# Performance work log

Hardware: AMD Instinct MI355X
Metric: run time of the kernel (lower is better)

## Reference

```python
import jax, jax.numpy as jnp
import numpy as np
from jax import lax

B, S, D, H, T = 128, 512, 128, 128, 20


def setup_inputs() -> dict:
    key = jax.random.key(0)
    ks = jax.random.split(key, 16)
    sc = 1.0 / np.sqrt(H)
    u = lambda k, shape: jax.random.uniform(k, shape, jnp.float32, -sc, sc)
    return {
        "inputs": jax.random.normal(ks[0], (B, S, D), jnp.float32),
        "tags": jax.random.randint(ks[1], (B, S), 0, T),
        "mask": jnp.ones((B, S), jnp.bool_),
        "w_ih_f": u(ks[2], (4 * H, D)),
        "w_hh_f": u(ks[3], (4 * H, H)),
        "b_f": u(ks[4], (4 * H,)),
        "w_ih_b": u(ks[5], (4 * H, D)),
        "w_hh_b": u(ks[6], (4 * H, H)),
        "b_b": u(ks[7], (4 * H,)),
        "w_out": u(ks[8], (T, 2 * H)),
        "b_out": u(ks[9], (T,)),
        "start_trans": jax.random.uniform(ks[10], (T,), jnp.float32, -0.1, 0.1),
        "end_trans": jax.random.uniform(ks[11], (T,), jnp.float32, -0.1, 0.1),
        "trans": jax.random.uniform(ks[12], (T, T), jnp.float32, -0.1, 0.1),
    }


def _lstm_dir(x, w_ih, w_hh, b, reverse):
    # x: [B,S,D] -> hidden states [B,S,H]
    xp = jnp.einsum('bsd,gd->bsg', x, w_ih) + b  # precomputed input gates [B,S,4H]
    if reverse:
        xp = xp[:, ::-1]
    h0 = jnp.zeros((x.shape[0], H), x.dtype)
    c0 = jnp.zeros((x.shape[0], H), x.dtype)

    def step(carry, xt):
        h, c = carry
        g = xt + h @ w_hh.T
        i, f, gg, o = jnp.split(g, 4, axis=-1)
        i, f, o = jax.nn.sigmoid(i), jax.nn.sigmoid(f), jax.nn.sigmoid(o)
        c = f * c + i * jnp.tanh(gg)
        h = o * jnp.tanh(c)
        return (h, c), h

    _, hs = lax.scan(step, (h0, c0), xp.transpose(1, 0, 2))
    hs = hs.transpose(1, 0, 2)  # [B,S,H]
    if reverse:
        hs = hs[:, ::-1]
    return hs


def _crf_nll(em, tags, mask, start_trans, end_trans, trans):
    # em: [B,S,T]; torchcrf log-likelihood, reduction='mean', negated
    b, s, t = em.shape
    maskf = mask.astype(em.dtype)
    batch = jnp.arange(b)
    # numerator: score of the gold path
    num = start_trans[tags[:, 0]] + em[batch, 0, tags[:, 0]]
    em_tag = jnp.take_along_axis(em, tags[:, :, None], axis=2)[:, :, 0]  # [B,S]
    trans_tag = trans[tags[:, :-1], tags[:, 1:]]  # [B,S-1]
    num = num + jnp.sum((trans_tag + em_tag[:, 1:]) * maskf[:, 1:], axis=1)
    seq_ends = jnp.sum(mask.astype(jnp.int32), axis=1) - 1
    num = num + end_trans[tags[batch, seq_ends]]
    # denominator: forward algorithm (logsumexp semiring) via scan
    score0 = start_trans[None, :] + em[:, 0]  # [B,T]

    def step(score, inp):
        em_t, m_t = inp
        nxt = jax.nn.logsumexp(score[:, :, None] + trans[None] + em_t[:, None, :], axis=1)
        return jnp.where(m_t[:, None], nxt, score), None

    score, _ = lax.scan(step, score0, (em[:, 1:].transpose(1, 0, 2), mask[:, 1:].T))
    den = jax.nn.logsumexp(score + end_trans[None, :], axis=1)
    return -jnp.mean(num - den)


def reference(inputs, tags, mask, w_ih_f, w_hh_f, b_f, w_ih_b, w_hh_b, b_b,
              w_out, b_out, start_trans, end_trans, trans):
    h_f = _lstm_dir(inputs, w_ih_f, w_hh_f, b_f, reverse=False)
    h_b = _lstm_dir(inputs, w_ih_b, w_hh_b, b_b, reverse=True)
    lstm_out = jnp.concatenate([h_f, h_b], axis=-1)  # [B,S,2H]
    emissions = jnp.einsum('bsh,th->bst', lstm_out, w_out) + b_out  # [B,S,T]
    return _crf_nll(emissions, tags, mask, start_trans, end_trans, trans)
```

## Files before the change

### kernel.cpp

```cpp
#include <hip/hip_runtime.h>
#include <cstdint>
#include <cstddef>

#define DEVINL __device__ __forceinline__

constexpr int Bz = 128, Sl = 512, Dm = 128, Hd = 128, NC = 1024, Tt = 20;
constexpr int Mrows = Bz * Sl;

constexpr size_t OFF_XP   = 17043456;
constexpr size_t OFF_HS   = 151261184;
constexpr size_t OFF_PART = 190058496;

DEVINL unsigned short f2bf(float f) {
    uint32_t u = __float_as_uint(f);
    u += 0x7fffu + ((u >> 16) & 1u);
    return (unsigned short)(u >> 16);
}
DEVINL float bf2f(unsigned short h) { return __uint_as_float(((uint32_t)h) << 16); }

DEVINL float rcpf(float x) { return __builtin_amdgcn_rcpf(x); }

DEVINL void barrier_lds_only() {
    __asm__ __volatile__("s_waitcnt lgkmcnt(0)" ::: "memory");
    __builtin_amdgcn_s_barrier();
    __asm__ __volatile__("" ::: "memory");
}

template <int CTRL>
DEVINL float qperm(float v) {
    int i = __float_as_int(v);
    int r = __builtin_amdgcn_update_dpp(i, i, CTRL, 0xF, 0xF, true);
    return __int_as_float(r);
}

typedef __attribute__((ext_vector_type(8))) __bf16 bf16x8;
typedef __attribute__((ext_vector_type(4))) float f32x4;
typedef _Float16 __attribute__((ext_vector_type(2))) half2_t;
typedef _Float16 __attribute__((ext_vector_type(8))) half8_t;

__global__ __launch_bounds__(256) void gemm_xp_k(
    const float* __restrict__ X, const float* __restrict__ wihf, const float* __restrict__ wihb,
    const float* __restrict__ b_f, const float* __restrict__ b_b,
    unsigned short* __restrict__ xp)
{
    __shared__ __align__(16) unsigned short As[128 * 72];
    __shared__ __align__(16) unsigned short Bs[128 * 72];
    const int m0 = blockIdx.x * 128, n0 = blockIdx.y * 128;
    const float* Bsrc = (n0 < 512) ? (wihf + (size_t)n0 * 128) : (wihb + (size_t)(n0 - 512) * 128);
    const int tid = threadIdx.x;
    const int wave = tid >> 6, lane = tid & 63;
    const int wm = (wave >> 1) * 64, wn = (wave & 1) * 64;
    const int ln = lane & 15, qd = lane >> 4;
    const int colc = (tid & 15) * 4, rowb = tid >> 4;

    f32x4 acc[4][4] = {};
    for (int ks = 0; ks < 2; ++ks) {
        const int k0 = ks * 64;
        __syncthreads();
        #pragma unroll
        for (int r = 0; r < 8; ++r) {
            int row = rowb + r * 16;
            float4 av = *(const float4*)(&X[(size_t)(m0 + row) * 128 + k0 + colc]);
            float4 bv = *(const float4*)(&Bsrc[(size_t)row * 128 + k0 + colc]);
            ushort4 au; au.x = f2bf(av.x); au.y = f2bf(av.y); au.z = f2bf(av.z); au.w = f2bf(av.w);
            ushort4 bu; bu.x = f2bf(bv.x); bu.y = f2bf(bv.y); bu.z = f2bf(bv.z); bu.w = f2bf(bv.w);
            *(ushort4*)(&As[row * 72 + colc]) = au;
            *(ushort4*)(&Bs[row * 72 + colc]) = bu;
        }
        __syncthreads();
        #pragma unroll
        for (int kk = 0; kk < 2; ++kk) {
            const int kb = kk * 32 + qd * 8;
            bf16x8 af[4], bfr[4];
            #pragma unroll
            for (int i = 0; i < 4; ++i) {
                af[i]  = *(const bf16x8*)(&As[(wm + i * 16 + ln) * 72 + kb]);
                bfr[i] = *(const bf16x8*)(&Bs[(wn + i * 16 + ln) * 72 + kb]);
            }
            #pragma unroll
            for (int i = 0; i < 4; ++i)
                #pragma unroll
                for (int j = 0; j < 4; ++j)
                    acc[i][j] = __builtin_amdgcn_mfma_f32_16x16x32_bf16(af[i], bfr[j], acc[i][j], 0, 0, 0);
        }
    }
    #pragma unroll
    for (int j = 0; j < 4; ++j) {
        const int col = n0 + wn + j * 16 + ln;
        const float bv = (col < 512) ? b_f[col] : b_b[col - 512];
        #pragma unroll
        for (int i = 0; i < 4; ++i) {
            const int rowg = m0 + wm + i * 16 + qd * 4;
            const int bidx = rowg >> 9, tloc = rowg & 511;
            ushort4 o;
            o.x = f2bf(acc[i][j][0] + bv); o.y = f2bf(acc[i][j][1] + bv);
            o.z = f2bf(acc[i][j][2] + bv); o.w = f2bf(acc[i][j][3] + bv);
            *(ushort4*)(xp + ((size_t)bidx * 1024 + col) * 512 + tloc) = o;
        }
    }
}

__global__ __launch_bounds__(512, 1) void lstm_k(
    const float* __restrict__ whf, const float* __restrict__ whb,
    const unsigned short* __restrict__ xp, unsigned short* __restrict__ hs)
{
    __shared__ __align__(16) _Float16 h_buf[2][128];
    const int dir = blockIdx.x >> 7;
    const int b   = blockIdx.x & 127;
    const int tid = threadIdx.x;
    const int lane = tid & 63;
    const int wv   = tid >> 6;
    const int q    = lane & 3;
    const int u    = wv * 16 + (lane >> 2);
    const int grow = q * 128 + u;

    const float* wsrc = dir ? whb : whf;
    half2_t w2[4][16];
    #pragma unroll
    for (int g = 0; g < 4; ++g) {
        const float* wrow = wsrc + (size_t)(g * 128 + u) * 128 + q * 32;
        #pragma unroll
        for (int k = 0; k < 16; ++k)
            w2[g][k] = half2_t{(_Float16)wrow[2 * k], (_Float16)wrow[2 * k + 1]};
    }

    const float S  = (q == 2) ? 2.f : 1.f;
    const float Aa = (q == 2) ? 2.f : 1.f;
    const float Bc = (q == 2) ? -1.f : 0.f;

    if (tid < 128) { h_buf[0][tid] = (_Float16)0.f; h_buf[1][tid] = (_Float16)0.f; }
    __syncthreads();

    const unsigned short* xrow = xp + ((size_t)b * 1024 + dir * 512 + grow) * 512;
    unsigned short* hptr = hs + (size_t)dir * Mrows * 128 + (size_t)b * Sl * 128 + u
                              + (dir ? (size_t)(Sl - 1) * 128 : 0);
    const int hstep = dir ? -128 : 128;

    float c = 0.f;
    ushort4 cur;
    {
        ushort4 r = *(const ushort4*)(xrow + (dir ? 508 : 0));
        cur = dir ? ushort4{r.w, r.z, r.y, r.x} : r;
    }

    for (int t = 0; t < Sl; t += 4) {
        const int tn = (t + 4 < Sl) ? (t + 4) : 0;
        ushort4 nraw = *(const ushort4*)(xrow + (dir ? (508 - tn) : tn));

        #pragma unroll
        for (int s = 0; s < 4; ++s) {
            const int p = s & 1;
            const unsigned short xb = (s == 0) ? cur.x : (s == 1) ? cur.y : (s == 2) ? cur.z : cur.w;
            float xv = bf2f(xb);

            const half8_t* hp = (const half8_t*)&h_buf[p][q * 32];
            float p0 = 0.f, p1 = 0.f, p2 = 0.f, p3 = 0.f;
            #pragma unroll
            for (int k = 0; k < 4; ++k) {
                half8_t hv = hp[k];
                const half2_t* h2 = (const half2_t*)&hv;
                #pragma unroll
                for (int j = 0; j < 4; ++j) {
                    p0 = __builtin_amdgcn_fdot2(w2[0][4 * k + j], h2[j], p0, false);
                    p1 = __builtin_amdgcn_fdot2(w2[1][4 * k + j], h2[j], p1, false);
                    p2 = __builtin_amdgcn_fdot2(w2[2][4 * k + j], h2[j], p2, false);
                    p3 = __builtin_amdgcn_fdot2(w2[3][4 * k + j], h2[j], p3, false);
                }
            }
            float keep0 = (q & 1) ? p1 : p0;
            float send0 = (q & 1) ? p0 : p1;
            float keep1 = (q & 1) ? p3 : p2;
            float send1 = (q & 1) ? p2 : p3;
            float s0 = keep0 + qperm<0xB1>(send0);
            float s1 = keep1 + qperm<0xB1>(send1);
            float keep2 = (q & 2) ? s1 : s0;
            float send2 = (q & 2) ? s0 : s1;
            float tot = keep2 + qperm<0x4E>(send2) + xv;

            float act = Aa * rcpf(1.f + __expf(-S * tot)) + Bc;
            float a0 = qperm<0x00>(act);
            float a1 = qperm<0x55>(act);
            float a2 = qperm<0xAA>(act);
            float a3 = qperm<0xFF>(act);
            c = fmaf(a1, c, a0 * a2);
            float th = 1.f - 2.f * rcpf(1.f + __expf(2.f * c));
            float h = a3 * th;
            if (q == 0) {
                _Float16 hh = (_Float16)h;
                h_buf[1 - p][u] = hh;
                unsigned short hbits; __builtin_memcpy(&hbits, &hh, 2);
                *hptr = hbits;
            }
            hptr += hstep;
            barrier_lds_only();
        }
        cur = dir ? ushort4{nraw.w, nraw.z, nraw.y, nraw.x} : nraw;
    }
}

__global__ __launch_bounds__(320, 1) void emcrf_k(
    const unsigned short* __restrict__ hs, const float* __restrict__ wout,
    const float* __restrict__ bout, const int* __restrict__ tags,
    const float* __restrict__ st, const float* __restrict__ et,
    const float* __restrict__ trans, float* __restrict__ part)
{
    __shared__ float em_s[Sl * Tt];
    __shared__ float red[320];
    const int b = blockIdx.x, tid = threadIdx.x, lane = tid & 63;
    const int* tg = tags + (size_t)b * Sl;

    {
        const int tag  = tid % 20;
        const int copy = tid / 20;
        const float* wr = wout + (size_t)tag * 256;
        half2_t wreg[128];
        #pragma unroll
        for (int k = 0; k < 128; ++k)
            wreg[k] = half2_t{(_Float16)wr[2 * k], (_Float16)wr[2 * k + 1]};
        const float bo = bout[tag];
        const unsigned short* hf_base = hs + (size_t)b * Sl * 128;
        const unsigned short* hb_base = hs + (size_t)Mrows * 128 + (size_t)b * Sl * 128;
        for (int i = 0; i < 32; ++i) {
            const int t = copy + 16 * i;
            const uint4* hf4 = (const uint4*)(hf_base + (size_t)t * 128);
            const uint4* hb4 = (const uint4*)(hb_base + (size_t)t * 128);
            float a0 = bo, a1 = 0.f, a2 = 0.f, a3 = 0.f;
            #pragma unroll
            for (int k = 0; k < 16; ++k) {
                uint4 v = hf4[k];
                half2_t h2[4]; __builtin_memcpy(h2, &v, 16);
                a0 = __builtin_amdgcn_fdot2(wreg[4 * k + 0], h2[0], a0, false);
                a1 = __builtin_amdgcn_fdot2(wreg[4 * k + 1], h2[1], a1, false);
                a2 = __builtin_amdgcn_fdot2(wreg[4 * k + 2], h2[2], a2, false);
                a3 = __builtin_amdgcn_fdot2(wreg[4 * k + 3], h2[3], a3, false);
            }
            #pragma unroll
            for (int k = 0; k < 16; ++k) {
                uint4 v = hb4[k];
                half2_t h2[4]; __builtin_memcpy(h2, &v, 16);
                a0 = __builtin_amdgcn_fdot2(wreg[64 + 4 * k + 0], h2[0], a0, false);
                a1 = __builtin_amdgcn_fdot2(wreg[64 + 4 * k + 1], h2[1], a1, false);
                a2 = __builtin_amdgcn_fdot2(wreg[64 + 4 * k + 2], h2[2], a2, false);
                a3 = __builtin_amdgcn_fdot2(wreg[64 + 4 * k + 3], h2[3], a3, false);
            }
            em_s[t * 20 + tag] = (a0 + a1) + (a2 + a3);
        }
    }
    __syncthreads();

    float nacc = 0.f;
    for (int t = 1 + tid; t < Sl; t += 320) {
        int tp = tg[t - 1], tc = tg[t];
        nacc += trans[tp * Tt + tc] + em_s[t * 20 + tc];
    }
    red[tid] = nacc;
    __syncthreads();

    if (tid < 64) {
        float v = red[lane] + red[lane + 64] + red[lane + 128] + red[lane + 192] + red[lane + 256];
        #pragma unroll
        for (int off = 32; off; off >>= 1) v += __shfl_down(v, off);

        float Etr[20];
        #pragma unroll
        for (int i = 0; i < 20; ++i)
            Etr[i] = (lane < 20) ? __expf(trans[i * Tt + lane]) : 0.f;

        float C = 0.f;
        float p = (lane < 20) ? __expf(st[lane] + em_s[lane]) : 0.f;
        float ev1 = (lane < 20) ? em_s[1 * 20 + lane] : 0.f;
        float ev2 = (lane < 20) ? em_s[2 * 20 + lane] : 0.f;
        for (int t = 1; t < Sl; ++t) {
            float ev = ev1;
            ev1 = ev2;
            int tn = t + 2 < Sl ? t + 2 : Sl - 1;
            ev2 = (lane < 20) ? em_s[tn * 20 + lane] : 0.f;

            float q0 = 0.f, q1 = 0.f, q2 = 0.f, q3 = 0.f;
            #pragma unroll
            for (int i = 0; i < 20; i += 4) {
                q0 = fmaf(__int_as_float(__builtin_amdgcn_readlane(__float_as_int(p), i + 0)), Etr[i + 0], q0);
                q1 = fmaf(__int_as_float(__builtin_amdgcn_readlane(__float_as_int(p), i + 1)), Etr[i + 1], q1);
                q2 = fmaf(__int_as_float(__builtin_amdgcn_readlane(__float_as_int(p), i + 2)), Etr[i + 2], q2);
                q3 = fmaf(__int_as_float(__builtin_amdgcn_readlane(__float_as_int(p), i + 3)), Etr[i + 3], q3);
            }
            p = ((q0 + q1) + (q2 + q3)) * __expf(ev);
            if ((t & 3) == 0) {
                float S0 = 0.f, S1 = 0.f, S2 = 0.f, S3 = 0.f;
                #pragma unroll
                for (int i = 0; i < 20; i += 4) {
                    S0 += __int_as_float(__builtin_amdgcn_readlane(__float_as_int(p), i + 0));
                    S1 += __int_as_float(__builtin_amdgcn_readlane(__float_as_int(p), i + 1));
                    S2 += __int_as_float(__builtin_amdgcn_readlane(__float_as_int(p), i + 2));
                    S3 += __int_as_float(__builtin_amdgcn_readlane(__float_as_int(p), i + 3));
                }
                float Ssum = (S0 + S1) + (S2 + S3);
                C += __logf(Ssum);
                p *= rcpf(Ssum);
            }
        }
        float f = (lane < 20) ? p * __expf(et[lane]) : 0.f;
        float S0 = 0.f, S1 = 0.f, S2 = 0.f, S3 = 0.f;
        #pragma unroll
        for (int i = 0; i < 20; i += 4) {
            S0 += __int_as_float(__builtin_amdgcn_readlane(__float_as_int(f), i + 0));
            S1 += __int_as_float(__builtin_amdgcn_readlane(__float_as_int(f), i + 1));
            S2 += __int_as_float(__builtin_amdgcn_readlane(__float_as_int(f), i + 2));
            S3 += __int_as_float(__builtin_amdgcn_readlane(__float_as_int(f), i + 3));
        }
        float den = C + __logf((S0 + S1) + (S2 + S3));
        if (lane == 0)
            part[b] = v + st[tg[0]] + em_s[tg[0]] + et[tg[Sl - 1]] - den;
    }
}

__global__ void fin_k(const float* __restrict__ part, float* __restrict__ out) {
    int l = threadIdx.x;
    float v = part[l] + part[l + 64];
    #pragma unroll
    for (int off = 32; off; off >>= 1) v += __shfl_xor(v, off);
    if (l == 0) out[0] = -v * (1.f / 128.f);
}

extern "C" void kernel_launch(void* const* d_in, const int* in_sizes, int n_in,
                              void* d_out, int out_size, void* d_ws, size_t ws_size,
                              hipStream_t stream) {
    const float* x      = (const float*)d_in[0];
    const int*   tags   = (const int*)d_in[1];
    const float* w_ih_f = (const float*)d_in[3];
    const float* w_hh_f = (const float*)d_in[4];
    const float* b_f    = (const float*)d_in[5];
    const float* w_ih_b = (const float*)d_in[6];
    const float* w_hh_b = (const float*)d_in[7];
    const float* b_b    = (const float*)d_in[8];
    const float* w_out  = (const float*)d_in[9];
    const float* b_out  = (const float*)d_in[10];
    const float* st     = (const float*)d_in[11];
    const float* et     = (const float*)d_in[12];
    const float* trans  = (const float*)d_in[13];
    float* out = (float*)d_out;

    char* ws = (char*)d_ws;
    unsigned short* xp   = (unsigned short*)(ws + OFF_XP);
    unsigned short* hs   = (unsigned short*)(ws + OFF_HS);
    float*          part = (float*)(ws + OFF_PART);

    gemm_xp_k<<<dim3(Mrows / 128, NC / 128), 256, 0, stream>>>(x, w_ih_f, w_ih_b, b_f, b_b, xp);
    lstm_k<<<256, 512, 0, stream>>>(w_hh_f, w_hh_b, xp, hs);
    emcrf_k<<<Bz, 320, 0, stream>>>(hs, w_out, b_out, tags, st, et, trans, part);
    fin_k<<<1, 64, 0, stream>>>(part, out);
}
```

Measured before the change: 553.1 us.

## Split emission and CRF kernels, restructure input GEMM to reuse A tile

The input-projection GEMM now loads each 64-row X tile once and loops over all eight 128-column weight tiles, instead of launching a 2D grid that reloads X per column tile. The fused emission+CRF kernel is split in two. The emission kernel runs 4 blocks per batch element, stages w_out through LDS and writes emissions to a global buffer. A single-wave CRF kernel then reads them with an 8-deep register prefetch. This spreads the emission dot products across more CUs and removes the 320-thread block that sat mostly idle during the serial CRF scan, at the cost of a global round-trip for emissions and an extra launch.

```diff
diff --git a/kernel.cpp b/kernel.cpp
--- a/kernel.cpp
+++ b/kernel.cpp
@@ -9,6 +9,7 @@
 
 constexpr size_t OFF_XP   = 17043456;
 constexpr size_t OFF_HS   = 151261184;
+constexpr size_t OFF_EM   = 184815616;
 constexpr size_t OFF_PART = 190058496;
 
 DEVINL unsigned short f2bf(float f) {
@@ -38,64 +39,73 @@
 typedef _Float16 __attribute__((ext_vector_type(2))) half2_t;
 typedef _Float16 __attribute__((ext_vector_type(8))) half8_t;
 
-__global__ __launch_bounds__(256) void gemm_xp_k(
+__global__ __launch_bounds__(256, 2) void gemm_xp_k(
     const float* __restrict__ X, const float* __restrict__ wihf, const float* __restrict__ wihb,
     const float* __restrict__ b_f, const float* __restrict__ b_b,
     unsigned short* __restrict__ xp)
 {
-    __shared__ __align__(16) unsigned short As[128 * 72];
-    __shared__ __align__(16) unsigned short Bs[128 * 72];
-    const int m0 = blockIdx.x * 128, n0 = blockIdx.y * 128;
-    const float* Bsrc = (n0 < 512) ? (wihf + (size_t)n0 * 128) : (wihb + (size_t)(n0 - 512) * 128);
+    __shared__ __align__(16) unsigned short As[64 * 132];
+    __shared__ __align__(16) unsigned short Bs[128 * 132];
+    const int m0 = blockIdx.x * 64;
     const int tid = threadIdx.x;
     const int wave = tid >> 6, lane = tid & 63;
-    const int wm = (wave >> 1) * 64, wn = (wave & 1) * 64;
+    const int wm = (wave >> 1) * 32, wn = (wave & 1) * 64;
     const int ln = lane & 15, qd = lane >> 4;
-    const int colc = (tid & 15) * 4, rowb = tid >> 4;
-
-    f32x4 acc[4][4] = {};
-    for (int ks = 0; ks < 2; ++ks) {
-        const int k0 = ks * 64;
+    const int colc = (tid & 31) * 4, rowb = tid >> 5;
+
+    #pragma unroll
+    for (int r = 0; r < 8; ++r) {
+        int row = rowb + r * 8;
+        float4 av = *(const float4*)(&X[(size_t)(m0 + row) * 128 + colc]);
+        ushort4 au; au.x = f2bf(av.x); au.y = f2bf(av.y); au.z = f2bf(av.z); au.w = f2bf(av.w);
+        *(ushort4*)(&As[row * 132 + colc]) = au;
+    }
+
+    const int bidx = m0 >> 9;
+    const int tbase = m0 & 511;
+
+    for (int nt = 0; nt < 8; ++nt) {
+        const float* Bsrc = (nt < 4) ? (wihf + (size_t)nt * 128 * 128)
+                                     : (wihb + (size_t)(nt - 4) * 128 * 128);
         __syncthreads();
         #pragma unroll
-        for (int r = 0; r < 8; ++r) {
-            int row = rowb + r * 16;
-            float4 av = *(const float4*)(&X[(size_t)(m0 + row) * 128 + k0 + colc]);
-            float4 bv = *(const float4*)(&Bsrc[(size_t)row * 128 + k0 + colc]);
-            ushort4 au; au.x = f2bf(av.x); au.y = f2bf(av.y); au.z = f2bf(av.z); au.w = f2bf(av.w);
+        for (int r = 0; r < 16; ++r) {
+            int row = rowb + r * 8;
+            float4 bv = *(const float4*)(&Bsrc[(size_t)row * 128 + colc]);
             ushort4 bu; bu.x = f2bf(bv.x); bu.y = f2bf(bv.y); bu.z = f2bf(bv.z); bu.w = f2bf(bv.w);
-            *(ushort4*)(&As[row * 72 + colc]) = au;
-            *(ushort4*)(&Bs[row * 72 + colc]) = bu;
+            *(ushort4*)(&Bs[row * 132 + colc]) = bu;
         }
         __syncthreads();
-        #pragma unroll
-        for (int kk = 0; kk < 2; ++kk) {
+
+        f32x4 acc[2][4] = {};
+        #pragma unroll
+        for (int kk = 0; kk < 4; ++kk) {
             const int kb = kk * 32 + qd * 8;
-            bf16x8 af[4], bfr[4];
-            #pragma unroll
-            for (int i = 0; i < 4; ++i) {
-                af[i]  = *(const bf16x8*)(&As[(wm + i * 16 + ln) * 72 + kb]);
-                bfr[i] = *(const bf16x8*)(&Bs[(wn + i * 16 + ln) * 72 + kb]);
-            }
-            #pragma unroll
-            for (int i = 0; i < 4; ++i)
+            bf16x8 af[2], bfr[4];
+            #pragma unroll
+            for (int i = 0; i < 2; ++i)
+                af[i] = *(const bf16x8*)(&As[(wm + i * 16 + ln) * 132 + kb]);
+            #pragma unroll
+            for (int j = 0; j < 4; ++j)
+                bfr[j] = *(const bf16x8*)(&Bs[(wn + j * 16 + ln) * 132 + kb]);
+            #pragma unroll
+            for (int i = 0; i < 2; ++i)
                 #pragma unroll
                 for (int j = 0; j < 4; ++j)
                     acc[i][j] = __builtin_amdgcn_mfma_f32_16x16x32_bf16(af[i], bfr[j], acc[i][j], 0, 0, 0);
         }
-    }
-    #pragma unroll
-    for (int j = 0; j < 4; ++j) {
-        const int col = n0 + wn + j * 16 + ln;
-        const float bv = (col < 512) ? b_f[col] : b_b[col - 512];
-        #pragma unroll
-        for (int i = 0; i < 4; ++i) {
-            const int rowg = m0 + wm + i * 16 + qd * 4;
-            const int bidx = rowg >> 9, tloc = rowg & 511;
-            ushort4 o;
-            o.x = f2bf(acc[i][j][0] + bv); o.y = f2bf(acc[i][j][1] + bv);
-            o.z = f2bf(acc[i][j][2] + bv); o.w = f2bf(acc[i][j][3] + bv);
-            *(ushort4*)(xp + ((size_t)bidx * 1024 + col) * 512 + tloc) = o;
+        #pragma unroll
+        for (int j = 0; j < 4; ++j) {
+            const int col = nt * 128 + wn + j * 16 + ln;
+            const float bv = (col < 512) ? b_f[col] : b_b[col - 512];
+            #pragma unroll
+            for (int i = 0; i < 2; ++i) {
+                const int tloc = tbase + wm + i * 16 + qd * 4;
+                ushort4 o;
+                o.x = f2bf(acc[i][j][0] + bv); o.y = f2bf(acc[i][j][1] + bv);
+                o.z = f2bf(acc[i][j][2] + bv); o.w = f2bf(acc[i][j][3] + bv);
+                *(ushort4*)(xp + ((size_t)bidx * 1024 + col) * 512 + tloc) = o;
+            }
         }
     }
 }
@@ -198,120 +208,143 @@
     }
 }
 
-__global__ __launch_bounds__(320, 1) void emcrf_k(
+__global__ __launch_bounds__(320, 1) void emis_k(
     const unsigned short* __restrict__ hs, const float* __restrict__ wout,
-    const float* __restrict__ bout, const int* __restrict__ tags,
+    const float* __restrict__ bout, float* __restrict__ em)
+{
+    __shared__ __align__(16) half2_t wlds[20 * 128];
+    const int b  = blockIdx.x >> 2;
+    const int qt = blockIdx.x & 3;
+    const int tid = threadIdx.x;
+
+    #pragma unroll
+    for (int k = 0; k < 8; ++k) {
+        int i = tid + k * 320;
+        wlds[i] = half2_t{(_Float16)wout[2 * i], (_Float16)wout[2 * i + 1]};
+    }
+    __syncthreads();
+
+    const int tag  = tid % 20;
+    const int copy = tid / 20;
+    half2_t wreg[128];
+    {
+        const uint4* wl4 = (const uint4*)&wlds[tag * 128];
+        #pragma unroll
+        for (int k = 0; k < 32; ++k) {
+            uint4 v = wl4[k];
+            __builtin_memcpy(&wreg[4 * k], &v, 16);
+        }
+    }
+    const float bo = bout[tag];
+    const unsigned short* hf_base = hs + (size_t)b * Sl * 128;
+    const unsigned short* hb_base = hs + (size_t)Mrows * 128 + (size_t)b * Sl * 128;
+
+    #pragma unroll
+    for (int i = 0; i < 8; ++i) {
+        const int t = qt * 128 + copy + 16 * i;
+        const uint4* hf4 = (const uint4*)(hf_base + (size_t)t * 128);
+        const uint4* hb4 = (const uint4*)(hb_base + (size_t)t * 128);
+        float a0 = bo, a1 = 0.f, a2 = 0.f, a3 = 0.f;
+        #pragma unroll
+        for (int k = 0; k < 16; ++k) {
+            uint4 v = hf4[k];
+            half2_t h2[4]; __builtin_memcpy(h2, &v, 16);
+            a0 = __builtin_amdgcn_fdot2(wreg[4 * k + 0], h2[0], a0, false);
+            a1 = __builtin_amdgcn_fdot2(wreg[4 * k + 1], h2[1], a1, false);
+            a2 = __builtin_amdgcn_fdot2(wreg[4 * k + 2], h2[2], a2, false);
+            a3 = __builtin_amdgcn_fdot2(wreg[4 * k + 3], h2[3], a3, false);
+        }
+        #pragma unroll
+        for (int k = 0; k < 16; ++k) {
+            uint4 v = hb4[k];
+            half2_t h2[4]; __builtin_memcpy(h2, &v, 16);
+            a0 = __builtin_amdgcn_fdot2(wreg[64 + 4 * k + 0], h2[0], a0, false);
+            a1 = __builtin_amdgcn_fdot2(wreg[64 + 4 * k + 1], h2[1], a1, false);
+            a2 = __builtin_amdgcn_fdot2(wreg[64 + 4 * k + 2], h2[2], a2, false);
+            a3 = __builtin_amdgcn_fdot2(wreg[64 + 4 * k + 3], h2[3], a3, false);
+        }
+        em[((size_t)b * Sl + t) * Tt + tag] = (a0 + a1) + (a2 + a3);
+    }
+}
+
+__global__ __launch_bounds__(64) void crf_k(
+    const float* __restrict__ em, const int* __restrict__ tags,
     const float* __restrict__ st, const float* __restrict__ et,
     const float* __restrict__ trans, float* __restrict__ part)
 {
-    __shared__ float em_s[Sl * Tt];
-    __shared__ float red[320];
-    const int b = blockIdx.x, tid = threadIdx.x, lane = tid & 63;
+    const int b = blockIdx.x, lane = threadIdx.x;
+    const float* emb = em + (size_t)b * Sl * Tt;
     const int* tg = tags + (size_t)b * Sl;
 
-    {
-        const int tag  = tid % 20;
-        const int copy = tid / 20;
-        const float* wr = wout + (size_t)tag * 256;
-        half2_t wreg[128];
-        #pragma unroll
-        for (int k = 0; k < 128; ++k)
-            wreg[k] = half2_t{(_Float16)wr[2 * k], (_Float16)wr[2 * k + 1]};
-        const float bo = bout[tag];
-        const unsigned short* hf_base = hs + (size_t)b * Sl * 128;
-        const unsigned short* hb_base = hs + (size_t)Mrows * 128 + (size_t)b * Sl * 128;
-        for (int i = 0; i < 32; ++i) {
-            const int t = copy + 16 * i;
-            const uint4* hf4 = (const uint4*)(hf_base + (size_t)t * 128);
-            const uint4* hb4 = (const uint4*)(hb_base + (size_t)t * 128);
-            float a0 = bo, a1 = 0.f, a2 = 0.f, a3 = 0.f;
-            #pragma unroll
-            for (int k = 0; k < 16; ++k) {
-                uint4 v = hf4[k];
-                half2_t h2[4]; __builtin_memcpy(h2, &v, 16);
-                a0 = __builtin_amdgcn_fdot2(wreg[4 * k + 0], h2[0], a0, false);
-                a1 = __builtin_amdgcn_fdot2(wreg[4 * k + 1], h2[1], a1, false);
-                a2 = __builtin_amdgcn_fdot2(wreg[4 * k + 2], h2[2], a2, false);
-                a3 = __builtin_amdgcn_fdot2(wreg[4 * k + 3], h2[3], a3, false);
-            }
-            #pragma unroll
-            for (int k = 0; k < 16; ++k) {
-                uint4 v = hb4[k];
-                half2_t h2[4]; __builtin_memcpy(h2, &v, 16);
-                a0 = __builtin_amdgcn_fdot2(wreg[64 + 4 * k + 0], h2[0], a0, false);
-                a1 = __builtin_amdgcn_fdot2(wreg[64 + 4 * k + 1], h2[1], a1, false);
-                a2 = __builtin_amdgcn_fdot2(wreg[64 + 4 * k + 2], h2[2], a2, false);
-                a3 = __builtin_amdgcn_fdot2(wreg[64 + 4 * k + 3], h2[3], a3, false);
-            }
-            em_s[t * 20 + tag] = (a0 + a1) + (a2 + a3);
-        }
-    }
-    __syncthreads();
-
     float nacc = 0.f;
-    for (int t = 1 + tid; t < Sl; t += 320) {
+    for (int t = 1 + lane; t < Sl; t += 64) {
         int tp = tg[t - 1], tc = tg[t];
-        nacc += trans[tp * Tt + tc] + em_s[t * 20 + tc];
-    }
-    red[tid] = nacc;
-    __syncthreads();
-
-    if (tid < 64) {
-        float v = red[lane] + red[lane + 64] + red[lane + 128] + red[lane + 192] + red[lane + 256];
-        #pragma unroll
-        for (int off = 32; off; off >>= 1) v += __shfl_down(v, off);
-
-        float Etr[20];
-        #pragma unroll
-        for (int i = 0; i < 20; ++i)
-            Etr[i] = (lane < 20) ? __expf(trans[i * Tt + lane]) : 0.f;
-
-        float C = 0.f;
-        float p = (lane < 20) ? __expf(st[lane] + em_s[lane]) : 0.f;
-        float ev1 = (lane < 20) ? em_s[1 * 20 + lane] : 0.f;
-        float ev2 = (lane < 20) ? em_s[2 * 20 + lane] : 0.f;
-        for (int t = 1; t < Sl; ++t) {
-            float ev = ev1;
-            ev1 = ev2;
-            int tn = t + 2 < Sl ? t + 2 : Sl - 1;
-            ev2 = (lane < 20) ? em_s[tn * 20 + lane] : 0.f;
-
-            float q0 = 0.f, q1 = 0.f, q2 = 0.f, q3 = 0.f;
-            #pragma unroll
-            for (int i = 0; i < 20; i += 4) {
-                q0 = fmaf(__int_as_float(__builtin_amdgcn_readlane(__float_as_int(p), i + 0)), Etr[i + 0], q0);
-                q1 = fmaf(__int_as_float(__builtin_amdgcn_readlane(__float_as_int(p), i + 1)), Etr[i + 1], q1);
-                q2 = fmaf(__int_as_float(__builtin_amdgcn_readlane(__float_as_int(p), i + 2)), Etr[i + 2], q2);
-                q3 = fmaf(__int_as_float(__builtin_amdgcn_readlane(__float_as_int(p), i + 3)), Etr[i + 3], q3);
-            }
-            p = ((q0 + q1) + (q2 + q3)) * __expf(ev);
-            if ((t & 3) == 0) {
-                float S0 = 0.f, S1 = 0.f, S2 = 0.f, S3 = 0.f;
+        nacc += trans[tp * Tt + tc] + emb[t * Tt + tc];
+    }
+    #pragma unroll
+    for (int off = 32; off; off >>= 1) nacc += __shfl_down(nacc, off);
+
+    float Etr[20];
+    #pragma unroll
+    for (int i = 0; i < 20; ++i)
+        Etr[i] = (lane < 20) ? __expf(trans[i * Tt + lane]) : 0.f;
+
+    float C = 0.f;
+    float p = (lane < 20) ? __expf(st[lane] + emb[lane]) : 0.f;
+
+    float evr[8];
+    #pragma unroll
+    for (int s = 0; s < 8; ++s) {
+        int tt = 1 + s; tt = tt < Sl ? tt : Sl - 1;
+        evr[s] = (lane < 20) ? emb[(size_t)tt * Tt + lane] : 0.f;
+    }
+
+    for (int t0 = 1; t0 < Sl; t0 += 8) {
+        #pragma unroll
+        for (int s = 0; s < 8; ++s) {
+            const int t = t0 + s;
+            if (t < Sl) {
+                float ev = evr[s];
+                int tf = t + 8; tf = tf < Sl ? tf : Sl - 1;
+                evr[s] = (lane < 20) ? emb[(size_t)tf * Tt + lane] : 0.f;
+
+                float q0 = 0.f, q1 = 0.f, q2 = 0.f, q3 = 0.f;
                 #pragma unroll
                 for (int i = 0; i < 20; i += 4) {
-                    S0 += __int_as_float(__builtin_amdgcn_readlane(__float_as_int(p), i + 0));
-                    S1 += __int_as_float(__builtin_amdgcn_readlane(__float_as_int(p), i + 1));
-                    S2 += __int_as_float(__builtin_amdgcn_readlane(__float_as_int(p), i + 2));
-                    S3 += __int_as_float(__builtin_amdgcn_readlane(__float_as_int(p), i + 3));
+                    q0 = fmaf(__int_as_float(__builtin_amdgcn_readlane(__float_as_int(p), i + 0)), Etr[i + 0], q0);
+                    q1 = fmaf(__int_as_float(__builtin_amdgcn_readlane(__float_as_int(p), i + 1)), Etr[i + 1], q1);
+                    q2 = fmaf(__int_as_float(__builtin_amdgcn_readlane(__float_as_int(p), i + 2)), Etr[i + 2], q2);
+                    q3 = fmaf(__int_as_float(__builtin_amdgcn_readlane(__float_as_int(p), i + 3)), Etr[i + 3], q3);
                 }
-                float Ssum = (S0 + S1) + (S2 + S3);
-                C += __logf(Ssum);
-                p *= rcpf(Ssum);
+                p = ((q0 + q1) + (q2 + q3)) * __expf(ev);
+                if ((s & 3) == 3) {
+                    float S0 = 0.f, S1 = 0.f, S2 = 0.f, S3 = 0.f;
+                    #pragma unroll
+                    for (int i = 0; i < 20; i += 4) {
+                        S0 += __int_as_float(__builtin_amdgcn_readlane(__float_as_int(p), i + 0));
+                        S1 += __int_as_float(__builtin_amdgcn_readlane(__float_as_int(p), i + 1));
+                        S2 += __int_as_float(__builtin_amdgcn_readlane(__float_as_int(p), i + 2));
+                        S3 += __int_as_float(__builtin_amdgcn_readlane(__float_as_int(p), i + 3));
+                    }
+                    float Ssum = (S0 + S1) + (S2 + S3);
+                    C += __logf(Ssum);
+                    p *= rcpf(Ssum);
+                }
             }
         }
-        float f = (lane < 20) ? p * __expf(et[lane]) : 0.f;
-        float S0 = 0.f, S1 = 0.f, S2 = 0.f, S3 = 0.f;
-        #pragma unroll
-        for (int i = 0; i < 20; i += 4) {
-            S0 += __int_as_float(__builtin_amdgcn_readlane(__float_as_int(f), i + 0));
-            S1 += __int_as_float(__builtin_amdgcn_readlane(__float_as_int(f), i + 1));
-            S2 += __int_as_float(__builtin_amdgcn_readlane(__float_as_int(f), i + 2));
-            S3 += __int_as_float(__builtin_amdgcn_readlane(__float_as_int(f), i + 3));
-        }
-        float den = C + __logf((S0 + S1) + (S2 + S3));
-        if (lane == 0)
-            part[b] = v + st[tg[0]] + em_s[tg[0]] + et[tg[Sl - 1]] - den;
-    }
+    }
+    float f = (lane < 20) ? p * __expf(et[lane]) : 0.f;
+    float S0 = 0.f, S1 = 0.f, S2 = 0.f, S3 = 0.f;
+    #pragma unroll
+    for (int i = 0; i < 20; i += 4) {
+        S0 += __int_as_float(__builtin_amdgcn_readlane(__float_as_int(f), i + 0));
+        S1 += __int_as_float(__builtin_amdgcn_readlane(__float_as_int(f), i + 1));
+        S2 += __int_as_float(__builtin_amdgcn_readlane(__float_as_int(f), i + 2));
+        S3 += __int_as_float(__builtin_amdgcn_readlane(__float_as_int(f), i + 3));
+    }
+    float den = C + __logf((S0 + S1) + (S2 + S3));
+    if (lane == 0)
+        part[b] = nacc + st[tg[0]] + emb[tg[0]] + et[tg[Sl - 1]] - den;
 }
 
 __global__ void fin_k(const float* __restrict__ part, float* __restrict__ out) {
@@ -343,10 +376,12 @@
     char* ws = (char*)d_ws;
     unsigned short* xp   = (unsigned short*)(ws + OFF_XP);
     unsigned short* hs   = (unsigned short*)(ws + OFF_HS);
+    float*          em   = (float*)(ws + OFF_EM);
     float*          part = (float*)(ws + OFF_PART);
 
-    gemm_xp_k<<<dim3(Mrows / 128, NC / 128), 256, 0, stream>>>(x, w_ih_f, w_ih_b, b_f, b_b, xp);
+    gemm_xp_k<<<Mrows / 64, 256, 0, stream>>>(x, w_ih_f, w_ih_b, b_f, b_b, xp);
     lstm_k<<<256, 512, 0, stream>>>(w_hh_f, w_hh_b, xp, hs);
-    emcrf_k<<<Bz, 320, 0, stream>>>(hs, w_out, b_out, tags, st, et, trans, part);
+    emis_k<<<Bz * 4, 320, 0, stream>>>(hs, w_out, b_out, em);
+    crf_k<<<Bz, 64, 0, stream>>>(em, tags, st, et, trans, part);
     fin_k<<<1, 64, 0, stream>>>(part, out);
 }
```

Result: faster. 524.7 us (-5.1%).
